# Optimization experiments

Measured on AMD Instinct MI355X. Metric: run time of the kernel, lower is better.

Reference implementation:

```python
import jax, jax.numpy as jnp
import numpy as np

DIM = 1024
HEADS = 16
DIM_HEAD = 64
INNER = HEADS * DIM_HEAD  # 1024
EPS = 1e-5


def layer_norm(x, gamma, beta):
    mu = jnp.mean(x, axis=-1, keepdims=True)
    var = jnp.mean(jnp.square(x - mu), axis=-1, keepdims=True)
    return (x - mu) * jax.lax.rsqrt(var + EPS) * gamma + beta


def setup_inputs() -> dict:
    key = jax.random.key(0)
    ks = jax.random.split(key, 6)
    b, n1, n2 = 8, 4096, 256
    x = jax.random.normal(ks[0], (b, n1, DIM), dtype=jnp.float32)
    latents = jax.random.normal(ks[1], (b, n2, DIM), dtype=jnp.float32)
    s = 1.0 / np.sqrt(DIM)
    Wq = jax.random.normal(ks[2], (DIM, INNER), dtype=jnp.float32) * s
    Wkv = jax.random.normal(ks[3], (DIM, 2 * INNER), dtype=jnp.float32) * s
    Wout = jax.random.normal(ks[4], (INNER, DIM), dtype=jnp.float32) * (1.0 / np.sqrt(INNER))
    g1 = jnp.ones((DIM,), jnp.float32); b1 = jnp.zeros((DIM,), jnp.float32)
    g2 = jnp.ones((DIM,), jnp.float32); b2 = jnp.zeros((DIM,), jnp.float32)
    return {"x": x, "latents": latents, "g1": g1, "b1": b1, "g2": g2, "b2": b2,
            "Wq": Wq, "Wkv": Wkv, "Wout": Wout}


def reference(x, latents, g1, b1, g2, b2, Wq, Wkv, Wout):
    b, l, _ = latents.shape
    xn = layer_norm(x, g1, b1)
    ln = layer_norm(latents, g2, b2)
    q = ln @ Wq  # (b, n2, inner)
    kv_input = jnp.concatenate([xn, ln], axis=1)  # (b, n1+n2, D)
    kv = kv_input @ Wkv
    k, v = jnp.split(kv, 2, axis=-1)
    # split heads -> (b, h, len, dh)
    def heads(t):
        return t.reshape(t.shape[0], t.shape[1], HEADS, DIM_HEAD).transpose(0, 2, 1, 3)
    q, k, v = heads(q), heads(k), heads(v)
    scale = 1.0 / np.sqrt(np.sqrt(DIM_HEAD))
    logits = jnp.einsum('bhqd,bhkd->bhqk', q * scale, k * scale)
    w = jax.nn.softmax(logits.astype(jnp.float32), axis=-1).astype(logits.dtype)
    out = jnp.einsum('bhqk,bhkd->bhqd', w, v)
    out = out.transpose(0, 2, 1, 3).reshape(b, l, INNER)
    return out @ Wout
```

## Files before the change

kernel.cpp:

```cpp
#include <hip/hip_runtime.h>
#include <hip/hip_bf16.h>

#define NB 8
#define N1 4096
#define N2 256
#define DIMD 1024
#define HEADS 16
#define DHD 64
#define KVLEN 4352
#define EPSF 1e-5f
#define L2E 1.44269504088896340736f

typedef __bf16 bf16x8 __attribute__((ext_vector_type(8)));
typedef float f32x4 __attribute__((ext_vector_type(4)));

__device__ __forceinline__ unsigned short f2bf(float f) {
  union { float f; unsigned int u; } v; v.f = f;
  return (unsigned short)((v.u + 0x7FFFu + ((v.u >> 16) & 1u)) >> 16);
}

__device__ __forceinline__ void gload_lds16(const void* g, void* l) {
  __builtin_amdgcn_global_load_lds(
      (const __attribute__((address_space(1))) void*)g,
      (__attribute__((address_space(3))) void*)l, 16, 0, 0);
}

__global__ __launch_bounds__(256) void ln_kernel(
    const float* __restrict__ in, const float* __restrict__ g, const float* __restrict__ bt,
    unsigned short* __restrict__ out, int rows_per_b, int out_off)
{
  int row = blockIdx.x;
  int b = row / rows_per_b;
  int r = row - b * rows_per_b;
  long orow = (long)b * KVLEN + out_off + r;
  const float* rp = in + (long)row * DIMD;
  int t = threadIdx.x;

  float4 x = *reinterpret_cast<const float4*>(rp + t * 4);
  float s = x.x + x.y + x.z + x.w;
  #pragma unroll
  for (int off = 1; off < 64; off <<= 1) s += __shfl_xor(s, off);
  __shared__ float red[8];
  int w = t >> 6;
  if ((t & 63) == 0) red[w] = s;
  __syncthreads();
  float mean = (red[0] + red[1] + red[2] + red[3]) * (1.0f / DIMD);

  float dx = x.x - mean, dy = x.y - mean, dz = x.z - mean, dw = x.w - mean;
  float sq = dx * dx + dy * dy + dz * dz + dw * dw;
  #pragma unroll
  for (int off = 1; off < 64; off <<= 1) sq += __shfl_xor(sq, off);
  if ((t & 63) == 0) red[4 + w] = sq;
  __syncthreads();
  float var = (red[4] + red[5] + red[6] + red[7]) * (1.0f / DIMD);
  float rs = rsqrtf(var + EPSF);

  float4 gg = *reinterpret_cast<const float4*>(g + t * 4);
  float4 bb = *reinterpret_cast<const float4*>(bt + t * 4);
  ushort4 o;
  o.x = f2bf(dx * rs * gg.x + bb.x);
  o.y = f2bf(dy * rs * gg.y + bb.y);
  o.z = f2bf(dz * rs * gg.z + bb.z);
  o.w = f2bf(dw * rs * gg.w + bb.w);
  *reinterpret_cast<ushort4*>(out + orow * DIMD + t * 4) = o;
}

__global__ __launch_bounds__(256) void transpose_bf16(
    const float* __restrict__ in, unsigned short* __restrict__ out, int R, int C)
{
  __shared__ float t[32][33];
  int r0 = blockIdx.y * 32, c0 = blockIdx.x * 32;
  int tx = threadIdx.x, ty = threadIdx.y;
  #pragma unroll
  for (int p = 0; p < 4; p++)
    t[ty + p * 8][tx] = in[(long)(r0 + ty + p * 8) * C + c0 + tx];
  __syncthreads();
  #pragma unroll
  for (int p = 0; p < 4; p++)
    out[(long)(c0 + ty + p * 8) * R + r0 + tx] = f2bf(t[tx][ty + p * 8]);
}


#define BARRIER8() { __builtin_amdgcn_sched_barrier(0); __builtin_amdgcn_s_barrier(); __builtin_amdgcn_sched_barrier(0); }
#define VMW4() { asm volatile("s_waitcnt vmcnt(4)" ::: "memory"); __builtin_amdgcn_sched_barrier(0); }

#define STG1(KIND, BUF, HALF, TILE, Q) \
  gload_lds16((KIND ? BT : A) + \
      (long)(((KIND) ? n0 : m0) + (HALF)*128 + w*16 + (Q)*8 + srow8) * 1024 + (TILE)*64 + sslot*8, \
      lds + (KIND)*32768 + (BUF)*16384 + ((HALF)*128 + w*16 + (Q)*8)*64)
#define STAGE8(KIND, BUF, HALF, TILE) { STG1(KIND,BUF,HALF,TILE,0); STG1(KIND,BUF,HALF,TILE,1); }

#define LDA8(BUF) { _Pragma("unroll") for (int mt = 0; mt < 8; mt++) { \
    int ar = wm*128 + mt*16 + lrow; \
    af[mt][0] = *(const bf16x8*)&lds[(BUF)*16384 + ar*64 + ((l4) ^ (ar&7))*8]; \
    af[mt][1] = *(const bf16x8*)&lds[(BUF)*16384 + ar*64 + ((4+l4) ^ (ar&7))*8]; } }

#define LDB8(BUF, NT) { int br = wn*64 + (NT)*16 + lrow; \
    bf0 = *(const bf16x8*)&lds[32768 + (BUF)*16384 + br*64 + ((l4) ^ (br&7))*8]; \
    bf1 = *(const bf16x8*)&lds[32768 + (BUF)*16384 + br*64 + ((4+l4) ^ (br&7))*8]; }

#define MM8(NT) { __builtin_amdgcn_s_setprio(1); \
    _Pragma("unroll") for (int mt = 0; mt < 8; mt++) { \
      acc[mt][NT] = __builtin_amdgcn_mfma_f32_16x16x32_bf16(af[mt][0], bf0, acc[mt][NT], 0, 0, 0); \
      acc[mt][NT] = __builtin_amdgcn_mfma_f32_16x16x32_bf16(af[mt][1], bf1, acc[mt][NT], 0, 0, 0); } \
    __builtin_amdgcn_s_setprio(0); }

__global__ __launch_bounds__(512, 1) void gemm8(
    const unsigned short* __restrict__ A, const unsigned short* __restrict__ BT,
    unsigned short* __restrict__ kbuf, unsigned short* __restrict__ vtbuf)
{
  __shared__ unsigned short lds[65536];
  int tid = threadIdx.x, l = tid & 63, w = tid >> 6;
  int wm = w >> 2, wn = w & 3;
  int lrow = l & 15, l4 = l >> 4;
  int bx = blockIdx.x, by = blockIdx.y;
  int m0 = by * 256, n0 = bx * 256;
  int srow8 = l >> 3;
  int sslot = (l & 7) ^ srow8;

  f32x4 acc[8][4] = {};
  bf16x8 af[8][2];
  bf16x8 bf0, bf1;

  STAGE8(0, 0, 0, 0); STAGE8(0, 0, 1, 0);
  STAGE8(1, 0, 0, 0); STAGE8(1, 0, 1, 0);
  STAGE8(0, 1, 0, 1); STAGE8(0, 1, 1, 1);
  VMW4(); BARRIER8();

  for (int it = 0; it < 8; ++it) {
    int t1 = 2 * it + 1;
    int t2 = 2 * it + 2; if (t2 > 15) t2 = 15;
    int t3 = 2 * it + 3; if (t3 > 15) t3 = 15;
    LDA8(0); LDB8(0, 0);
    STAGE8(1, 1, 0, t1);
    BARRIER8(); MM8(0); BARRIER8();
    LDB8(0, 1);
    STAGE8(1, 1, 1, t1);
    BARRIER8(); MM8(1); BARRIER8();
    LDB8(0, 2);
    STAGE8(0, 0, 0, t2);
    BARRIER8(); MM8(2); BARRIER8();
    LDB8(0, 3);
    STAGE8(0, 0, 1, t2);
    BARRIER8(); MM8(3); VMW4(); BARRIER8();
    LDA8(1); LDB8(1, 0);
    STAGE8(1, 0, 0, t2);
    BARRIER8(); MM8(0); BARRIER8();
    LDB8(1, 1);
    STAGE8(1, 0, 1, t2);
    BARRIER8(); MM8(1); BARRIER8();
    LDB8(1, 2);
    STAGE8(0, 1, 0, t3);
    BARRIER8(); MM8(2); BARRIER8();
    LDB8(1, 3);
    STAGE8(0, 1, 1, t3);
    BARRIER8(); MM8(3); VMW4(); BARRIER8();
  }

  __syncthreads();

  int b = by / 17;
  int kk0 = m0 - b * KVLEN;

  if (n0 < DIMD) {
    #pragma unroll
    for (int mt = 0; mt < 8; mt++)
      #pragma unroll
      for (int nt = 0; nt < 4; nt++)
        #pragma unroll
        for (int r = 0; r < 4; r++) {
          int kk = kk0 + wm * 128 + mt * 16 + l4 * 4 + r;
          int h = bx * 4 + wn;
          int d = nt * 16 + lrow;
          kbuf[(((long)(b * HEADS + h) * KVLEN + kk) << 6) + d] = f2bf(acc[mt][nt][r]);
        }
  } else {
    #pragma unroll
    for (int mt = 0; mt < 8; mt++)
      #pragma unroll
      for (int nt = 0; nt < 4; nt++)
        #pragma unroll
        for (int r = 0; r < 4; r++) {
          int nl = wn * 64 + nt * 16 + lrow;
          int ml = wm * 128 + mt * 16 + l4 * 4 + r;
          lds[nl * 256 + (ml ^ ((nl & 15) << 4))] = f2bf(acc[mt][nt][r]);
        }
    __syncthreads();
    int nl = tid >> 1, mc = (tid & 1) * 128;
    int h = bx * 4 + (nl >> 6) - HEADS;
    int d = nl & 63;
    unsigned short* op = vtbuf + ((long)(b * HEADS + h) * DHD + d) * KVLEN + kk0 + mc;
    #pragma unroll
    for (int j = 0; j < 16; j++) {
      bf16x8 v = *(const bf16x8*)&lds[nl * 256 + ((mc + j * 8) ^ ((nl & 15) << 4))];
      *(bf16x8*)(op + j * 8) = v;
    }
  }
}

__global__ __launch_bounds__(256) void gemm3(
    const unsigned short* __restrict__ A, const unsigned short* __restrict__ BT,
    int mode, unsigned short* __restrict__ obf, float* __restrict__ of32)
{
  __shared__ unsigned short As[128 * 32];
  __shared__ unsigned short Bs[64 * 32];
  const int K = DIMD;
  int tid = threadIdx.x, l = tid & 63, w = tid >> 6;
  int m0 = blockIdx.y * 128, n0 = blockIdx.x * 64;
  int lrow = l & 15, lk = (l >> 4) * 8;

  int sr = l >> 2, scol = (l & 3) * 8;
  long am0 = m0 + w * 16 + sr, am1 = m0 + (w + 4) * 16 + sr;
  if (mode == 0) {
    am0 = (am0 >> 8) * KVLEN + N1 + (am0 & 255);
    am1 = (am1 >> 8) * KVLEN + N1 + (am1 & 255);
  }
  const unsigned short* gA0 = A + am0 * K + scol;
  const unsigned short* gA1 = A + am1 * K + scol;
  const unsigned short* gB = BT + (long)(n0 + w * 16 + sr) * K + scol;
  unsigned short* lA0 = As + w * 512;
  unsigned short* lA1 = As + (w + 4) * 512;
  unsigned short* lB = Bs + w * 512;

  f32x4 acc[2][4] = {};

  for (int k0 = 0; k0 < K; k0 += 32) {
    gload_lds16(gA0, lA0);
    gload_lds16(gA1, lA1);
    gload_lds16(gB, lB);
    gA0 += 32; gA1 += 32; gB += 32;
    __syncthreads();
    bf16x8 af[2], bfr[4];
    #pragma unroll
    for (int i = 0; i < 2; i++)
      af[i] = *reinterpret_cast<bf16x8*>(&As[(w * 32 + i * 16 + lrow) * 32 + lk]);
    #pragma unroll
    for (int j = 0; j < 4; j++)
      bfr[j] = *reinterpret_cast<bf16x8*>(&Bs[(j * 16 + lrow) * 32 + lk]);
    #pragma unroll
    for (int i = 0; i < 2; i++)
      #pragma unroll
      for (int j = 0; j < 4; j++)
        acc[i][j] = __builtin_amdgcn_mfma_f32_16x16x32_bf16(af[i], bfr[j], acc[i][j], 0, 0, 0);
    __syncthreads();
  }

  #pragma unroll
  for (int i = 0; i < 2; i++)
    #pragma unroll
    for (int j = 0; j < 4; j++)
      #pragma unroll
      for (int r = 0; r < 4; r++) {
        int m = m0 + w * 32 + i * 16 + (l >> 4) * 4 + r;
        int n = n0 + j * 16 + lrow;
        float v = acc[i][j][r];
        if (mode == 0) {
          int b = m >> 8, qq = m & 255, h = n >> 6, d = n & 63;
          obf[(((long)(b * HEADS + h) * N2 + qq) << 6) + d] = f2bf(v * 0.125f);
        } else {
          of32[(long)m * DIMD + n] = v;
        }
      }
}

__global__ __launch_bounds__(256) void attn_kernel(
    const unsigned short* __restrict__ qb, const unsigned short* __restrict__ kb,
    const unsigned short* __restrict__ vtb, unsigned short* __restrict__ attn)
{
  __shared__ unsigned short Ks[64][72];
  __shared__ unsigned short Vs[64][72];
  __shared__ unsigned short Ps[4][16][72];
  int qt = blockIdx.x, bh = blockIdx.y;
  int tid = threadIdx.x, l = tid & 63, w = tid >> 6;
  int lrow = l & 15, lk = (l >> 4) * 8;

  const unsigned short* qp = qb + ((long)bh * N2 + qt * 64 + w * 16) * DHD;
  const unsigned short* kp = kb + (long)bh * KVLEN * DHD;
  const unsigned short* vp = vtb + (long)bh * DHD * KVLEN;

  bf16x8 qa[2];
  qa[0] = *reinterpret_cast<const bf16x8*>(qp + lrow * DHD + lk);
  qa[1] = *reinterpret_cast<const bf16x8*>(qp + lrow * DHD + 32 + lk);

  f32x4 O[4] = {};
  float mrow[4] = {-1e30f, -1e30f, -1e30f, -1e30f};
  float lsum[4] = {0.f, 0.f, 0.f, 0.f};

  for (int blk = 0; blk < KVLEN / 64; blk++) {
    __syncthreads();
    #pragma unroll
    for (int p = 0; p < 2; p++) {
      int eo = (tid + p * 256) * 8;
      int row = eo >> 6, col = eo & 63;
      *reinterpret_cast<bf16x8*>(&Ks[row][col]) =
          *reinterpret_cast<const bf16x8*>(kp + (long)(blk * 64 + row) * DHD + col);
      *reinterpret_cast<bf16x8*>(&Vs[row][col]) =
          *reinterpret_cast<const bf16x8*>(vp + (long)row * KVLEN + blk * 64 + col);
    }
    __syncthreads();

    f32x4 S[4];
    __builtin_amdgcn_s_setprio(1);
    #pragma unroll
    for (int nt = 0; nt < 4; nt++) {
      f32x4 s = {};
      #pragma unroll
      for (int kt = 0; kt < 2; kt++) {
        bf16x8 bk = *reinterpret_cast<bf16x8*>(&Ks[nt * 16 + lrow][kt * 32 + lk]);
        s = __builtin_amdgcn_mfma_f32_16x16x32_bf16(qa[kt], bk, s, 0, 0, 0);
      }
      S[nt] = s;
    }
    __builtin_amdgcn_s_setprio(0);

    float mx[4], rsum[4];
    #pragma unroll
    for (int r = 0; r < 4; r++) {
      float v = fmaxf(fmaxf(S[0][r], S[1][r]), fmaxf(S[2][r], S[3][r]));
      #pragma unroll
      for (int off = 1; off < 16; off <<= 1) v = fmaxf(v, __shfl_xor(v, off));
      mx[r] = v;
    }
    float fac[4];
    #pragma unroll
    for (int r = 0; r < 4; r++) {
      float mn = fmaxf(mrow[r], mx[r]);
      fac[r] = exp2f((mrow[r] - mn) * L2E);
      mrow[r] = mn;
      rsum[r] = 0.f;
    }
    #pragma unroll
    for (int nt = 0; nt < 4; nt++)
      #pragma unroll
      for (int r = 0; r < 4; r++) {
        float p = exp2f((S[nt][r] - mrow[r]) * L2E);
        rsum[r] += p;
        Ps[w][(l >> 4) * 4 + r][nt * 16 + lrow] = f2bf(p);
      }
    #pragma unroll
    for (int r = 0; r < 4; r++) {
      float v = rsum[r];
      #pragma unroll
      for (int off = 1; off < 16; off <<= 1) v += __shfl_xor(v, off);
      lsum[r] = lsum[r] * fac[r] + v;
    }
    #pragma unroll
    for (int dt = 0; dt < 4; dt++)
      #pragma unroll
      for (int r = 0; r < 4; r++) O[dt][r] *= fac[r];

    asm volatile("s_waitcnt lgkmcnt(0)" ::: "memory");
    bf16x8 pa[2];
    pa[0] = *reinterpret_cast<bf16x8*>(&Ps[w][lrow][lk]);
    pa[1] = *reinterpret_cast<bf16x8*>(&Ps[w][lrow][32 + lk]);
    __builtin_amdgcn_s_setprio(1);
    #pragma unroll
    for (int dt = 0; dt < 4; dt++)
      #pragma unroll
      for (int kt = 0; kt < 2; kt++) {
        bf16x8 bv = *reinterpret_cast<bf16x8*>(&Vs[dt * 16 + lrow][kt * 32 + lk]);
        O[dt] = __builtin_amdgcn_mfma_f32_16x16x32_bf16(pa[kt], bv, O[dt], 0, 0, 0);
      }
    __builtin_amdgcn_s_setprio(0);
  }

  int b = bh >> 4, h = bh & 15;
  #pragma unroll
  for (int dt = 0; dt < 4; dt++)
    #pragma unroll
    for (int r = 0; r < 4; r++) {
      int grow = b * N2 + qt * 64 + w * 16 + (l >> 4) * 4 + r;
      int col = h * DHD + dt * 16 + lrow;
      attn[(long)grow * DIMD + col] = f2bf(O[dt][r] / lsum[r]);
    }
}

extern "C" void kernel_launch(void* const* d_in, const int* in_sizes, int n_in,
                              void* d_out, int out_size, void* d_ws, size_t ws_size,
                              hipStream_t stream) {
  const float* x    = (const float*)d_in[0];
  const float* lat  = (const float*)d_in[1];
  const float* g1   = (const float*)d_in[2];
  const float* b1   = (const float*)d_in[3];
  const float* g2   = (const float*)d_in[4];
  const float* b2   = (const float*)d_in[5];
  const float* Wq   = (const float*)d_in[6];
  const float* Wkv  = (const float*)d_in[7];
  const float* Wout = (const float*)d_in[8];
  float* out = (float*)d_out;

  char* ws = (char*)d_ws;
  size_t off = 0;
  auto alloc = [&](size_t bytes) -> void* {
    void* p = ws + off;
    off += (bytes + 255) & ~(size_t)255;
    return p;
  };
  unsigned short* kvin  = (unsigned short*)alloc((size_t)NB * KVLEN * DIMD * 2);
  unsigned short* WqT   = (unsigned short*)alloc((size_t)DIMD * DIMD * 2);
  unsigned short* WkvT  = (unsigned short*)alloc((size_t)2 * DIMD * DIMD * 2);
  unsigned short* WoutT = (unsigned short*)alloc((size_t)DIMD * DIMD * 2);
  unsigned short* qbuf  = (unsigned short*)alloc((size_t)NB * N2 * DIMD * 2);
  unsigned short* kbuf  = (unsigned short*)alloc((size_t)NB * HEADS * KVLEN * DHD * 2);
  unsigned short* vtbuf = (unsigned short*)alloc((size_t)NB * HEADS * KVLEN * DHD * 2);
  unsigned short* attn  = (unsigned short*)alloc((size_t)NB * N2 * DIMD * 2);
  if (off > ws_size) return;

  transpose_bf16<<<dim3(DIMD / 32, DIMD / 32), dim3(32, 8), 0, stream>>>(Wq, WqT, DIMD, DIMD);
  transpose_bf16<<<dim3(2 * DIMD / 32, DIMD / 32), dim3(32, 8), 0, stream>>>(Wkv, WkvT, DIMD, 2 * DIMD);
  transpose_bf16<<<dim3(DIMD / 32, DIMD / 32), dim3(32, 8), 0, stream>>>(Wout, WoutT, DIMD, DIMD);

  ln_kernel<<<NB * N1, 256, 0, stream>>>(x, g1, b1, kvin, N1, 0);
  ln_kernel<<<NB * N2, 256, 0, stream>>>(lat, g2, b2, kvin, N2, N1);

  gemm3<<<dim3(16, 16), 256, 0, stream>>>(kvin, WqT, 0, qbuf, nullptr);
  gemm8<<<dim3(8, 136), 512, 0, stream>>>(kvin, WkvT, kbuf, vtbuf);
  attn_kernel<<<dim3(4, NB * HEADS), 256, 0, stream>>>(qbuf, kbuf, vtbuf, attn);
  gemm3<<<dim3(16, 16), 256, 0, stream>>>(attn, WoutT, 2, nullptr, out);
}
```

Baseline: 645.5 us.

## Restructure KV GEMM fragment loads, stage K output via LDS, double-buffer attention KV

The KV GEMM main loop now loads all B fragments once per k-tile and splits the A fragments into two halves, removing the sched barriers and replacing them with explicit lgkmcnt waits. The K-output epilogue goes through a swizzled LDS tile so stores to global memory are 16-byte vectors instead of scattered 2-byte writes. The attention kernel double-buffers K/V tiles in LDS, prefetching the next block into registers while computing the current one, which removes one barrier per iteration. It also remaps block IDs so neighbouring workgroups spread across batch-heads. The aim is better load/compute overlap and store coalescing, at the cost of more registers and LDS and a riskier instruction schedule.

```diff
diff --git a/kernel.cpp b/kernel.cpp
--- a/kernel.cpp
+++ b/kernel.cpp
@@ -81,7 +81,8 @@
 }
 
 
-#define BARRIER8() { __builtin_amdgcn_sched_barrier(0); __builtin_amdgcn_s_barrier(); __builtin_amdgcn_sched_barrier(0); }
+#define BAR8() __builtin_amdgcn_s_barrier()
+#define LGKM0() asm volatile("s_waitcnt lgkmcnt(0)" ::: "memory")
 #define VMW4() { asm volatile("s_waitcnt vmcnt(4)" ::: "memory"); __builtin_amdgcn_sched_barrier(0); }
 
 #define STG1(KIND, BUF, HALF, TILE, Q) \
@@ -90,20 +91,22 @@
       lds + (KIND)*32768 + (BUF)*16384 + ((HALF)*128 + w*16 + (Q)*8)*64)
 #define STAGE8(KIND, BUF, HALF, TILE) { STG1(KIND,BUF,HALF,TILE,0); STG1(KIND,BUF,HALF,TILE,1); }
 
-#define LDA8(BUF) { _Pragma("unroll") for (int mt = 0; mt < 8; mt++) { \
-    int ar = wm*128 + mt*16 + lrow; \
-    af[mt][0] = *(const bf16x8*)&lds[(BUF)*16384 + ar*64 + ((l4) ^ (ar&7))*8]; \
-    af[mt][1] = *(const bf16x8*)&lds[(BUF)*16384 + ar*64 + ((4+l4) ^ (ar&7))*8]; } }
-
-#define LDB8(BUF, NT) { int br = wn*64 + (NT)*16 + lrow; \
-    bf0 = *(const bf16x8*)&lds[32768 + (BUF)*16384 + br*64 + ((l4) ^ (br&7))*8]; \
-    bf1 = *(const bf16x8*)&lds[32768 + (BUF)*16384 + br*64 + ((4+l4) ^ (br&7))*8]; }
-
-#define MM8(NT) { __builtin_amdgcn_s_setprio(1); \
-    _Pragma("unroll") for (int mt = 0; mt < 8; mt++) { \
-      acc[mt][NT] = __builtin_amdgcn_mfma_f32_16x16x32_bf16(af[mt][0], bf0, acc[mt][NT], 0, 0, 0); \
-      acc[mt][NT] = __builtin_amdgcn_mfma_f32_16x16x32_bf16(af[mt][1], bf1, acc[mt][NT], 0, 0, 0); } \
-    __builtin_amdgcn_s_setprio(0); }
+#define LDB_ALL(BUF) { _Pragma("unroll") \
+  for (int nt = 0; nt < 4; nt++) { int br = wn*64 + nt*16 + lrow; \
+    bfr[nt][0] = *(const bf16x8*)&lds[32768 + (BUF)*16384 + br*64 + ((l4) ^ (br&7))*8]; \
+    bfr[nt][1] = *(const bf16x8*)&lds[32768 + (BUF)*16384 + br*64 + ((4+l4) ^ (br&7))*8]; } }
+
+#define LDA_H(BUF, AF, MT0) { _Pragma("unroll") \
+  for (int q = 0; q < 4; q++) { int ar = wm*128 + ((MT0)+q)*16 + lrow; \
+    AF[q][0] = *(const bf16x8*)&lds[(BUF)*16384 + ar*64 + ((l4) ^ (ar&7))*8]; \
+    AF[q][1] = *(const bf16x8*)&lds[(BUF)*16384 + ar*64 + ((4+l4) ^ (ar&7))*8]; } }
+
+#define MMP(AF, QB, MB) { __builtin_amdgcn_s_setprio(1); \
+  _Pragma("unroll") for (int q = 0; q < 2; q++) \
+    _Pragma("unroll") for (int nt = 0; nt < 4; nt++) { \
+      acc[(MB)+q][nt] = __builtin_amdgcn_mfma_f32_16x16x32_bf16(AF[(QB)+q][0], bfr[nt][0], acc[(MB)+q][nt], 0, 0, 0); \
+      acc[(MB)+q][nt] = __builtin_amdgcn_mfma_f32_16x16x32_bf16(AF[(QB)+q][1], bfr[nt][1], acc[(MB)+q][nt], 0, 0, 0); } \
+  __builtin_amdgcn_s_setprio(0); }
 
 __global__ __launch_bounds__(512, 1) void gemm8(
     const unsigned short* __restrict__ A, const unsigned short* __restrict__ BT,
@@ -119,42 +122,38 @@
   int sslot = (l & 7) ^ srow8;
 
   f32x4 acc[8][4] = {};
-  bf16x8 af[8][2];
-  bf16x8 bf0, bf1;
+  bf16x8 afA[4][2], afB[4][2];
+  bf16x8 bfr[4][2];
 
   STAGE8(0, 0, 0, 0); STAGE8(0, 0, 1, 0);
   STAGE8(1, 0, 0, 0); STAGE8(1, 0, 1, 0);
   STAGE8(0, 1, 0, 1); STAGE8(0, 1, 1, 1);
-  VMW4(); BARRIER8();
+  VMW4(); BAR8();
 
   for (int it = 0; it < 8; ++it) {
     int t1 = 2 * it + 1;
     int t2 = 2 * it + 2; if (t2 > 15) t2 = 15;
     int t3 = 2 * it + 3; if (t3 > 15) t3 = 15;
-    LDA8(0); LDB8(0, 0);
+    LDB_ALL(0); LDA_H(0, afA, 0);
     STAGE8(1, 1, 0, t1);
-    BARRIER8(); MM8(0); BARRIER8();
-    LDB8(0, 1);
+    BAR8(); LGKM0(); MMP(afA, 0, 0); BAR8();
+    LDA_H(0, afB, 4);
     STAGE8(1, 1, 1, t1);
-    BARRIER8(); MM8(1); BARRIER8();
-    LDB8(0, 2);
+    BAR8(); LGKM0(); MMP(afA, 2, 2); BAR8();
     STAGE8(0, 0, 0, t2);
-    BARRIER8(); MM8(2); BARRIER8();
-    LDB8(0, 3);
+    BAR8(); MMP(afB, 0, 4); BAR8();
     STAGE8(0, 0, 1, t2);
-    BARRIER8(); MM8(3); VMW4(); BARRIER8();
-    LDA8(1); LDB8(1, 0);
+    BAR8(); MMP(afB, 2, 6); VMW4(); BAR8();
+    LDB_ALL(1); LDA_H(1, afA, 0);
     STAGE8(1, 0, 0, t2);
-    BARRIER8(); MM8(0); BARRIER8();
-    LDB8(1, 1);
+    BAR8(); LGKM0(); MMP(afA, 0, 0); BAR8();
+    LDA_H(1, afB, 4);
     STAGE8(1, 0, 1, t2);
-    BARRIER8(); MM8(1); BARRIER8();
-    LDB8(1, 2);
+    BAR8(); LGKM0(); MMP(afA, 2, 2); BAR8();
     STAGE8(0, 1, 0, t3);
-    BARRIER8(); MM8(2); BARRIER8();
-    LDB8(1, 3);
+    BAR8(); MMP(afB, 0, 4); BAR8();
     STAGE8(0, 1, 1, t3);
-    BARRIER8(); MM8(3); VMW4(); BARRIER8();
+    BAR8(); MMP(afB, 2, 6); VMW4(); BAR8();
   }
 
   __syncthreads();
@@ -169,11 +168,19 @@
       for (int nt = 0; nt < 4; nt++)
         #pragma unroll
         for (int r = 0; r < 4; r++) {
-          int kk = kk0 + wm * 128 + mt * 16 + l4 * 4 + r;
-          int h = bx * 4 + wn;
-          int d = nt * 16 + lrow;
-          kbuf[(((long)(b * HEADS + h) * KVLEN + kk) << 6) + d] = f2bf(acc[mt][nt][r]);
+          int ml = wm * 128 + mt * 16 + l4 * 4 + r;
+          int nl = wn * 64 + nt * 16 + lrow;
+          lds[ml * 256 + (nl ^ ((ml & 15) << 4))] = f2bf(acc[mt][nt][r]);
         }
+    __syncthreads();
+    int ml = tid >> 1, nc = (tid & 1) * 128;
+    #pragma unroll
+    for (int j = 0; j < 16; j++) {
+      int nn = nc + j * 8;
+      int h = nn >> 6, d = nn & 63;
+      bf16x8 v = *(const bf16x8*)&lds[ml * 256 + (nn ^ ((ml & 15) << 4))];
+      *(bf16x8*)&kbuf[(((long)(b * HEADS + bx * 4 + h) * KVLEN + kk0 + ml) << 6) + d] = v;
+    }
   } else {
     #pragma unroll
     for (int mt = 0; mt < 8; mt++)
@@ -267,10 +274,12 @@
     const unsigned short* __restrict__ qb, const unsigned short* __restrict__ kb,
     const unsigned short* __restrict__ vtb, unsigned short* __restrict__ attn)
 {
-  __shared__ unsigned short Ks[64][72];
-  __shared__ unsigned short Vs[64][72];
+  __shared__ unsigned short Ks[2][64][72];
+  __shared__ unsigned short Vs[2][64][72];
   __shared__ unsigned short Ps[4][16][72];
-  int qt = blockIdx.x, bh = blockIdx.y;
+  int wgid = blockIdx.y * 4 + blockIdx.x;
+  int orig = (wgid & 7) * 64 + (wgid >> 3);
+  int qt = orig & 3, bh = orig >> 2;
   int tid = threadIdx.x, l = tid & 63, w = tid >> 6;
   int lrow = l & 15, lk = (l >> 4) * 8;
 
@@ -282,22 +291,33 @@
   qa[0] = *reinterpret_cast<const bf16x8*>(qp + lrow * DHD + lk);
   qa[1] = *reinterpret_cast<const bf16x8*>(qp + lrow * DHD + 32 + lk);
 
+  int krow = tid >> 3, kcol = (tid & 7) * 8;
+
   f32x4 O[4] = {};
   float mrow[4] = {-1e30f, -1e30f, -1e30f, -1e30f};
   float lsum[4] = {0.f, 0.f, 0.f, 0.f};
 
-  for (int blk = 0; blk < KVLEN / 64; blk++) {
+  bf16x8 kr0 = *(const bf16x8*)(kp + (long)krow * DHD + kcol);
+  bf16x8 kr1 = *(const bf16x8*)(kp + (long)(32 + krow) * DHD + kcol);
+  bf16x8 vr0 = *(const bf16x8*)(vp + (long)krow * KVLEN + kcol);
+  bf16x8 vr1 = *(const bf16x8*)(vp + (long)(32 + krow) * KVLEN + kcol);
+  *(bf16x8*)&Ks[0][krow][kcol] = kr0;
+  *(bf16x8*)&Ks[0][32 + krow][kcol] = kr1;
+  *(bf16x8*)&Vs[0][krow][kcol] = vr0;
+  *(bf16x8*)&Vs[0][32 + krow][kcol] = vr1;
+
+  const int NBLK = KVLEN / 64;
+  int cur = 0;
+  for (int blk = 0; blk < NBLK; blk++) {
     __syncthreads();
-    #pragma unroll
-    for (int p = 0; p < 2; p++) {
-      int eo = (tid + p * 256) * 8;
-      int row = eo >> 6, col = eo & 63;
-      *reinterpret_cast<bf16x8*>(&Ks[row][col]) =
-          *reinterpret_cast<const bf16x8*>(kp + (long)(blk * 64 + row) * DHD + col);
-      *reinterpret_cast<bf16x8*>(&Vs[row][col]) =
-          *reinterpret_cast<const bf16x8*>(vp + (long)row * KVLEN + blk * 64 + col);
-    }
-    __syncthreads();
+    if (blk + 1 < NBLK) {
+      const unsigned short* kn = kp + (long)((blk + 1) * 64) * DHD;
+      const unsigned short* vn = vp + (blk + 1) * 64;
+      kr0 = *(const bf16x8*)(kn + (long)krow * DHD + kcol);
+      kr1 = *(const bf16x8*)(kn + (long)(32 + krow) * DHD + kcol);
+      vr0 = *(const bf16x8*)(vn + (long)krow * KVLEN + kcol);
+      vr1 = *(const bf16x8*)(vn + (long)(32 + krow) * KVLEN + kcol);
+    }
 
     f32x4 S[4];
     __builtin_amdgcn_s_setprio(1);
@@ -306,7 +326,7 @@
       f32x4 s = {};
       #pragma unroll
       for (int kt = 0; kt < 2; kt++) {
-        bf16x8 bk = *reinterpret_cast<bf16x8*>(&Ks[nt * 16 + lrow][kt * 32 + lk]);
+        bf16x8 bk = *reinterpret_cast<bf16x8*>(&Ks[cur][nt * 16 + lrow][kt * 32 + lk]);
         s = __builtin_amdgcn_mfma_f32_16x16x32_bf16(qa[kt], bk, s, 0, 0, 0);
       }
       S[nt] = s;
@@ -358,10 +378,18 @@
     for (int dt = 0; dt < 4; dt++)
       #pragma unroll
       for (int kt = 0; kt < 2; kt++) {
-        bf16x8 bv = *reinterpret_cast<bf16x8*>(&Vs[dt * 16 + lrow][kt * 32 + lk]);
+        bf16x8 bv = *reinterpret_cast<bf16x8*>(&Vs[cur][dt * 16 + lrow][kt * 32 + lk]);
         O[dt] = __builtin_amdgcn_mfma_f32_16x16x32_bf16(pa[kt], bv, O[dt], 0, 0, 0);
       }
     __builtin_amdgcn_s_setprio(0);
+
+    if (blk + 1 < NBLK) {
+      *(bf16x8*)&Ks[cur ^ 1][krow][kcol] = kr0;
+      *(bf16x8*)&Ks[cur ^ 1][32 + krow][kcol] = kr1;
+      *(bf16x8*)&Vs[cur ^ 1][krow][kcol] = vr0;
+      *(bf16x8*)&Vs[cur ^ 1][32 + krow][kcol] = vr1;
+    }
+    cur ^= 1;
   }
 
   int b = bh >> 4, h = bh & 15;
```

Result: no change. 644.8 us (-0.1%).
